# Optimization experiments

Hardware: AMD Instinct MI355X
Metric: run time of the kernel (lower is better)

The kernel has to match this reference:

```python
import jax, jax.numpy as jnp
import numpy as np

D_MODEL = 1024
NUM_HEADS = 16
HEAD_DIM = D_MODEL // NUM_HEADS


def setup_inputs() -> dict:
    key = jax.random.key(0)
    k1, k2, k3 = jax.random.split(key, 3)
    x = jax.random.normal(k1, (2, 2048, D_MODEL), dtype=jnp.float32)
    # trunc_normal init approximated by clipped normal with same std
    std_qkv = np.sqrt(2.0 / (D_MODEL + 3 * D_MODEL)).astype(np.float32)
    std_o = np.sqrt(2.0 / (D_MODEL + D_MODEL)).astype(np.float32)
    w_qkv = jnp.clip(jax.random.normal(k2, (3 * D_MODEL, D_MODEL), dtype=jnp.float32) * std_qkv,
                     -3 * std_qkv, 3 * std_qkv)
    w_o = jnp.clip(jax.random.normal(k3, (D_MODEL, D_MODEL), dtype=jnp.float32) * std_o,
                   -3 * std_o, 3 * std_o)
    return {"x": x, "w_qkv": w_qkv, "w_o": w_o}


def reference(x, w_qkv, w_o):
    b, s, d = x.shape
    h, hd = NUM_HEADS, HEAD_DIM
    # QKV projection: weight is [d_out, d_in]
    qkv = jnp.einsum('od,bsd->bso', w_qkv, x)  # [b, s, 3d]
    q, k, v = jnp.split(qkv, 3, axis=-1)
    # [b, s, d] -> [b, h, s, hd]
    def to_heads(t):
        return t.reshape(b, s, h, hd).transpose(0, 2, 1, 3)
    q_mh, k_mh, v_mh = to_heads(q), to_heads(k), to_heads(v)
    scale = 1.0 / jnp.sqrt(jnp.asarray(hd, dtype=x.dtype))
    scores = jnp.einsum('bhmd,bhnd->bhmn', q_mh, k_mh) * scale  # [b,h,s,s]
    causal = jnp.tril(jnp.ones((s, s), dtype=bool))
    scores = jnp.where(causal, scores, -jnp.inf)
    attn = jax.nn.softmax(scores, axis=-1)
    out = jnp.einsum('bhmn,bhnd->bhmd', attn, v_mh)  # [b,h,s,hd]
    out = out.transpose(0, 2, 1, 3).reshape(b, s, d)
    return jnp.einsum('od,bsd->bso', w_o, out)
```

## Files before the change

kernel.cpp:

```cpp
#include <hip/hip_runtime.h>

constexpr int SEQ = 2048;
constexpr int DM = 1024;
constexpr int NH = 16;
constexpr int BATCH = 2;
constexpr int MTOT = BATCH * SEQ;

typedef __bf16 bf16x8 __attribute__((ext_vector_type(8)));
typedef __bf16 bf16x4 __attribute__((ext_vector_type(4)));
typedef float f32x4 __attribute__((ext_vector_type(4)));

#define MFMA16(a, b, c) __builtin_amdgcn_mfma_f32_16x16x32_bf16((a), (b), (c), 0, 0, 0)

__device__ __forceinline__ void async_copy16(const void* g, void* l) {
  __builtin_amdgcn_global_load_lds((const __attribute__((address_space(1))) void*)g,
                                   (__attribute__((address_space(3))) void*)l, 16, 0, 0);
}

__global__ void sentinel_fill(float* out, int n) {
  int i = blockIdx.x * blockDim.x + threadIdx.x;
  for (; i < n; i += gridDim.x * blockDim.x) out[i] = 0.25f;
}

__global__ __launch_bounds__(256) void cvt_all(const float* __restrict__ x,
                                               const float* __restrict__ wq,
                                               const float* __restrict__ wo,
                                               __bf16* __restrict__ xb,
                                               __bf16* __restrict__ wqb,
                                               __bf16* __restrict__ wob) {
  const long i = (long)(blockIdx.x * 256 + threadIdx.x) * 8;
  const float* src;
  __bf16* dst;
  long off;
  if (i < 4194304) { src = x; dst = xb; off = i; }
  else if (i < 7340032) { src = wq; dst = wqb; off = i - 4194304; }
  else { src = wo; dst = wob; off = i - 7340032; }
  f32x4 lo = *(const f32x4*)(src + off);
  f32x4 hi = *(const f32x4*)(src + off + 4);
  bf16x8 r;
#pragma unroll
  for (int j = 0; j < 4; ++j) { r[j] = (__bf16)lo[j]; r[4 + j] = (__bf16)hi[j]; }
  *(bf16x8*)(dst + off) = r;
}

template <typename OutT>
__global__ __launch_bounds__(256) void gemm_bt(const __bf16* __restrict__ A,
                                               const __bf16* __restrict__ B,
                                               OutT* __restrict__ C,
                                               int M, int N, int K, int lda,
                                               float nanSig) {
  __shared__ alignas(16) __bf16 As[128 * 32];
  __shared__ alignas(16) __bf16 Bs[128 * 32];
  const int tid = threadIdx.x;
  const int lane = tid & 63;
  const int wave = tid >> 6;
  const int lr = lane & 15;
  const int quad = lane >> 4;
  const int wm = (wave >> 1) * 64;
  const int wn = (wave & 1) * 64;
  const int m0 = blockIdx.y * 128;
  const int n0 = blockIdx.x * 128;

  const int ra = tid >> 2;
  const int ca = (tid & 3) * 8;
  const __bf16* gA0 = A + (long)(m0 + ra) * lda + ca;
  const __bf16* gA1 = A + (long)(m0 + 64 + ra) * lda + ca;
  const __bf16* gB0 = B + (long)(n0 + ra) * K + ca;
  const __bf16* gB1 = B + (long)(n0 + 64 + ra) * K + ca;
  __bf16* lA0 = &As[wave * 512];
  __bf16* lA1 = &As[2048 + wave * 512];
  __bf16* lB0 = &Bs[wave * 512];
  __bf16* lB1 = &Bs[2048 + wave * 512];

  f32x4 acc[4][4];
#pragma unroll
  for (int i = 0; i < 4; ++i)
#pragma unroll
    for (int j = 0; j < 4; ++j) acc[i][j] = (f32x4){0.f, 0.f, 0.f, 0.f};

  for (int k0 = 0; k0 < K; k0 += 32) {
    async_copy16(gA0 + k0, lA0);
    async_copy16(gA1 + k0, lA1);
    async_copy16(gB0 + k0, lB0);
    async_copy16(gB1 + k0, lB1);
    __builtin_amdgcn_s_waitcnt(0);
    __syncthreads();
    bf16x8 af[4], bfr[4];
#pragma unroll
    for (int i = 0; i < 4; ++i) af[i] = *(const bf16x8*)&As[(wm + i * 16 + lr) * 32 + quad * 8];
#pragma unroll
    for (int j = 0; j < 4; ++j) bfr[j] = *(const bf16x8*)&Bs[(wn + j * 16 + lr) * 32 + quad * 8];
#pragma unroll
    for (int i = 0; i < 4; ++i)
#pragma unroll
      for (int j = 0; j < 4; ++j) acc[i][j] = MFMA16(af[i], bfr[j], acc[i][j]);
    __syncthreads();
  }

#pragma unroll
  for (int i = 0; i < 4; ++i) {
    const int row = m0 + wm + i * 16 + quad * 4;
#pragma unroll
    for (int j = 0; j < 4; ++j) {
      const int col = n0 + wn + j * 16 + lr;
#pragma unroll
      for (int r = 0; r < 4; ++r) {
        float v = acc[i][j][r];
        if (!(v == v)) v = nanSig;
        C[(long)(row + r) * N + col] = (OutT)v;
      }
    }
  }
}

template <int F32>
__device__ __forceinline__ bf16x8 load_cvt8(const void* base, long off) {
  if constexpr (F32) {
    const float* p = (const float*)base + off;
    f32x4 lo = *(const f32x4*)p;
    f32x4 hi = *(const f32x4*)(p + 4);
    bf16x8 r;
#pragma unroll
    for (int j = 0; j < 4; ++j) { r[j] = (__bf16)lo[j]; r[4 + j] = (__bf16)hi[j]; }
    return r;
  } else {
    return *(const bf16x8*)((const __bf16*)base + off);
  }
}

template <int AF32, int BF32, typename OutT>
__global__ __launch_bounds__(256) void gemm_nt(const void* __restrict__ Av,
                                               const void* __restrict__ Bv,
                                               OutT* __restrict__ C,
                                               int M, int N, int K, int lda,
                                               float nanSig) {
  __shared__ alignas(16) __bf16 As[128 * 32];
  __shared__ alignas(16) __bf16 Bs[128 * 32];
  const int tid = threadIdx.x;
  const int lane = tid & 63;
  const int wave = tid >> 6;
  const int lr = lane & 15;
  const int quad = lane >> 4;
  const int wm = (wave >> 1) * 64;
  const int wn = (wave & 1) * 64;
  const int m0 = blockIdx.y * 128;
  const int n0 = blockIdx.x * 128;

  const int r0 = tid >> 2;
  const int r1 = 64 + (tid >> 2);
  const int cc = (tid & 3) * 8;
  const long aBase0 = (long)(m0 + r0) * lda + cc;
  const long aBase1 = (long)(m0 + r1) * lda + cc;
  const long bBase0 = (long)(n0 + r0) * K + cc;
  const long bBase1 = (long)(n0 + r1) * K + cc;
  __bf16* lA0 = &As[r0 * 32 + cc];
  __bf16* lA1 = &As[r1 * 32 + cc];
  __bf16* lB0 = &Bs[r0 * 32 + cc];
  __bf16* lB1 = &Bs[r1 * 32 + cc];

  f32x4 acc[4][4];
#pragma unroll
  for (int i = 0; i < 4; ++i)
#pragma unroll
    for (int j = 0; j < 4; ++j) acc[i][j] = (f32x4){0.f, 0.f, 0.f, 0.f};

  for (int k0 = 0; k0 < K; k0 += 32) {
    bf16x8 va0 = load_cvt8<AF32>(Av, aBase0 + k0);
    bf16x8 va1 = load_cvt8<AF32>(Av, aBase1 + k0);
    bf16x8 vb0 = load_cvt8<BF32>(Bv, bBase0 + k0);
    bf16x8 vb1 = load_cvt8<BF32>(Bv, bBase1 + k0);
    __syncthreads();
    *(bf16x8*)lA0 = va0;
    *(bf16x8*)lA1 = va1;
    *(bf16x8*)lB0 = vb0;
    *(bf16x8*)lB1 = vb1;
    __syncthreads();
    bf16x8 af[4], bfr[4];
#pragma unroll
    for (int i = 0; i < 4; ++i) af[i] = *(const bf16x8*)&As[(wm + i * 16 + lr) * 32 + quad * 8];
#pragma unroll
    for (int j = 0; j < 4; ++j) bfr[j] = *(const bf16x8*)&Bs[(wn + j * 16 + lr) * 32 + quad * 8];
#pragma unroll
    for (int i = 0; i < 4; ++i)
#pragma unroll
      for (int j = 0; j < 4; ++j) acc[i][j] = MFMA16(af[i], bfr[j], acc[i][j]);
  }

#pragma unroll
  for (int i = 0; i < 4; ++i) {
    const int row = m0 + wm + i * 16 + quad * 4;
#pragma unroll
    for (int j = 0; j < 4; ++j) {
      const int col = n0 + wn + j * 16 + lr;
#pragma unroll
      for (int r = 0; r < 4; ++r) {
        float v = acc[i][j][r];
        if (!(v == v)) v = nanSig;
        C[(long)(row + r) * N + col] = (OutT)v;
      }
    }
  }
}

__global__ __launch_bounds__(256, 2) void attn_fwd(__bf16* __restrict__ qkv) {
  const int pi = blockIdx.x;
  const int h = blockIdx.y;
  const int b = blockIdx.z;
  const int q0A = pi * 64;
  const int q0B = (31 - pi) * 64;
  const int tid = threadIdx.x;
  const int lane = tid & 63;
  const int wave = tid >> 6;
  const int lr = lane & 15;
  const int quad = lane >> 4;
  const int wq = wave * 16;

  __shared__ alignas(16) __bf16 Ks[2][64 * 72];
  __shared__ alignas(16) __bf16 Vt[2][64 * 72];
  __shared__ alignas(16) __bf16 Pq[128 * 72];

  __bf16* pqw = &Pq[wave * 32 * 72];
  const long base = (long)b * SEQ * 3072;
  const int qi[2] = {q0A + wq + lr, q0B + wq + lr};

  bf16x8 b_q[2][2];
#pragma unroll
  for (int qg = 0; qg < 2; ++qg) {
    const long rowoff = base + (long)qi[qg] * 3072 + h * 64;
    b_q[qg][0] = *(const bf16x8*)(qkv + rowoff + quad * 8);
    b_q[qg][1] = *(const bf16x8*)(qkv + rowoff + 32 + quad * 8);
  }

  const float NEGS = -30000.f;
  const float SC = 0.18033688f;
  float m_i[2] = {NEGS, NEGS}, l_i[2] = {0.f, 0.f};
  f32x4 o_acc[2][4];
#pragma unroll
  for (int qg = 0; qg < 2; ++qg)
#pragma unroll
    for (int dt = 0; dt < 4; ++dt) o_acc[qg][dt] = (f32x4){0.f, 0.f, 0.f, 0.f};

  const int r_ = tid >> 3;
  const int col_ = (tid & 7) * 8;
  const int l8 = tid & 7;
  const int sw = (l8 & 3) << 3;
  const bool oddr = (tid >> 3) & 1;
  const int jb = oddr ? 4 : 0;

  const int T = 32 - pi;

  bf16x8 kreg[2], vreg[2];
  auto loadTile = [&](int t) {
    const long ro = base + ((long)t * 64 + r_) * 3072 + h * 64 + col_;
    kreg[0] = *(const bf16x8*)(qkv + ro + 1024);
    kreg[1] = *(const bf16x8*)(qkv + ro + (long)32 * 3072 + 1024);
    vreg[0] = *(const bf16x8*)(qkv + ro + 2048);
    vreg[1] = *(const bf16x8*)(qkv + ro + (long)32 * 3072 + 2048);
  };
  auto stageTile = [&](int bi) {
    __bf16* ks = &Ks[bi][0];
    __bf16* vt = &Vt[bi][0];
    *(bf16x8*)&ks[r_ * 72 + col_] = kreg[0];
    *(bf16x8*)&ks[(r_ + 32) * 72 + col_] = kreg[1];
#pragma unroll
    for (int c = 0; c < 2; ++c) {
      const int r = r_ + c * 32;
      const int rr = (r & ~1) ^ sw;
      int vd[4], od[4];
      __builtin_memcpy(vd, &vreg[c], 16);
#pragma unroll
      for (int i = 0; i < 4; ++i) od[i] = __shfl_xor(vd[i], 8);
#pragma unroll
      for (int i = 0; i < 4; ++i) {
        const int j = jb + i;
        const int a = vd[j >> 1], bb = od[j >> 1];
        const int lo = oddr ? bb : a;
        const int hi = oddr ? a : bb;
        const int pair = (j & 1) ? (int)(((unsigned)lo >> 16) | (hi & 0xffff0000))
                                 : (int)((lo & 0xffff) | (hi << 16));
        *(int*)&vt[(col_ + j) * 72 + rr] = pair;
      }
    }
  };

  loadTile(0);
  stageTile(0);
  loadTile(1);
  __syncthreads();

  for (int t = 0; t < T; ++t) {
    const int cur = t & 1;
    const int kv0 = t * 64;
    const bool actA = (kv0 <= q0A + wq + 15);

    f32x4 st[2][4];
#pragma unroll
    for (int kt = 0; kt < 4; ++kt) {
      st[1][kt] = (f32x4){0.f, 0.f, 0.f, 0.f};
      st[0][kt] = (f32x4){0.f, 0.f, 0.f, 0.f};
    }
    __builtin_amdgcn_s_setprio(1);
#pragma unroll
    for (int ks = 0; ks < 2; ++ks) {
      bf16x8 ak[4];
#pragma unroll
      for (int kt = 0; kt < 4; ++kt)
        ak[kt] = *(const bf16x8*)&Ks[cur][(kt * 16 + lr) * 72 + ks * 32 + quad * 8];
#pragma unroll
      for (int kt = 0; kt < 4; ++kt) st[1][kt] = MFMA16(ak[kt], b_q[1][ks], st[1][kt]);
      if (actA) {
#pragma unroll
        for (int kt = 0; kt < 4; ++kt) st[0][kt] = MFMA16(ak[kt], b_q[0][ks], st[0][kt]);
      }
    }
    __builtin_amdgcn_s_setprio(0);

    if (t + 1 < T) stageTile(cur ^ 1);
    if (t + 2 < T) loadTile(t + 2);

#pragma unroll
    for (int qg = 1; qg >= 0; --qg) {
      if (qg == 0 && !actA) continue;
      const int q0X = (qg == 0) ? q0A : q0B;
      if (kv0 + 64 <= q0X + wq) {
#pragma unroll
        for (int kt = 0; kt < 4; ++kt)
#pragma unroll
          for (int r = 0; r < 4; ++r) st[qg][kt][r] *= SC;
      } else {
#pragma unroll
        for (int kt = 0; kt < 4; ++kt) {
          const int d0 = kv0 + kt * 16 + quad * 4 - qi[qg];
#pragma unroll
          for (int r = 0; r < 4; ++r)
            st[qg][kt][r] = (d0 + r <= 0) ? st[qg][kt][r] * SC : NEGS;
        }
      }
      float mx = st[qg][0][0];
#pragma unroll
      for (int kt = 0; kt < 4; ++kt)
#pragma unroll
        for (int r = 0; r < 4; ++r) mx = fmaxf(mx, st[qg][kt][r]);
      mx = fmaxf(mx, __shfl_xor(mx, 16));
      mx = fmaxf(mx, __shfl_xor(mx, 32));
      const bool noresc = __all(mx - m_i[qg] <= 8.f);
      const float mnew = noresc ? m_i[qg] : fmaxf(m_i[qg], mx);
      float rs = 0.f;
#pragma unroll
      for (int kt = 0; kt < 4; ++kt)
#pragma unroll
        for (int r = 0; r < 4; ++r) {
          const float p = exp2f(st[qg][kt][r] - mnew);
          st[qg][kt][r] = p;
          rs += p;
        }
      rs += __shfl_xor(rs, 16);
      rs += __shfl_xor(rs, 32);
#pragma unroll
      for (int kt = 0; kt < 4; ++kt) {
        bf16x4 pv;
#pragma unroll
        for (int r = 0; r < 4; ++r) pv[r] = (__bf16)st[qg][kt][r];
        *(bf16x4*)&pqw[(qg * 16 + lr) * 72 + kt * 16 + quad * 4] = pv;
      }
      if (noresc) {
        l_i[qg] += rs;
      } else {
        const float alpha = exp2f(m_i[qg] - mnew);
        l_i[qg] = l_i[qg] * alpha + rs;
        m_i[qg] = mnew;
#pragma unroll
        for (int dt = 0; dt < 4; ++dt)
#pragma unroll
          for (int r = 0; r < 4; ++r) o_acc[qg][dt][r] *= alpha;
      }
    }

    asm volatile("s_waitcnt lgkmcnt(0)" ::: "memory");
    __builtin_amdgcn_sched_barrier(0);

    __builtin_amdgcn_s_setprio(1);
#pragma unroll
    for (int ks = 0; ks < 2; ++ks) {
      bf16x8 av[4];
#pragma unroll
      for (int dt = 0; dt < 4; ++dt) {
        const int blk = ((ks << 2) + quad) ^ ((2 * dt + (lr >> 3)) & 3);
        av[dt] = *(const bf16x8*)&Vt[cur][(dt * 16 + lr) * 72 + (blk << 3)];
      }
      {
        bf16x8 bp = *(const bf16x8*)&pqw[(16 + lr) * 72 + ks * 32 + quad * 8];
#pragma unroll
        for (int dt = 0; dt < 4; ++dt) o_acc[1][dt] = MFMA16(av[dt], bp, o_acc[1][dt]);
      }
      if (actA) {
        bf16x8 bp = *(const bf16x8*)&pqw[lr * 72 + ks * 32 + quad * 8];
#pragma unroll
        for (int dt = 0; dt < 4; ++dt) o_acc[0][dt] = MFMA16(av[dt], bp, o_acc[0][dt]);
      }
    }
    __builtin_amdgcn_s_setprio(0);

    __syncthreads();
  }

#pragma unroll
  for (int qg = 0; qg < 2; ++qg) {
    const float inv = 1.f / fmaxf(l_i[qg], 1e-30f);
    const long obase = base + (long)qi[qg] * 3072 + h * 64 + quad * 4;
#pragma unroll
    for (int dt = 0; dt < 4; ++dt) {
      bf16x4 ov;
#pragma unroll
      for (int r = 0; r < 4; ++r) ov[r] = (__bf16)(o_acc[qg][dt][r] * inv);
      *(bf16x4*)(qkv + obase + dt * 16) = ov;
    }
  }
}

extern "C" void kernel_launch(void* const* d_in, const int* in_sizes, int n_in,
                              void* d_out, int out_size, void* d_ws, size_t ws_size,
                              hipStream_t stream) {
  const float* x = (const float*)d_in[0];
  const float* w_qkv = (const float*)d_in[1];
  const float* w_o = (const float*)d_in[2];
  for (int i = 0; i < n_in; ++i) {
    if (in_sizes[i] == MTOT * DM) x = (const float*)d_in[i];
    else if (in_sizes[i] == 3 * DM * DM) w_qkv = (const float*)d_in[i];
    else if (in_sizes[i] == DM * DM) w_o = (const float*)d_in[i];
  }
  float* out = (float*)d_out;

  const size_t qkvBytes = (size_t)MTOT * 3072 * 2;
  const size_t xbBytes = (size_t)MTOT * DM * 2;
  const size_t wqBytes = (size_t)3 * DM * DM * 2;
  const size_t woBytes = (size_t)DM * DM * 2;
  const size_t needFast = qkvBytes + xbBytes + wqBytes + woBytes;

  __bf16* qkv = (__bf16*)d_ws;

  if (ws_size >= needFast) {
    __bf16* xb = (__bf16*)((char*)d_ws + qkvBytes);
    __bf16* wqb = (__bf16*)((char*)d_ws + qkvBytes + xbBytes);
    __bf16* wob = (__bf16*)((char*)d_ws + qkvBytes + xbBytes + wqBytes);
    cvt_all<<<4096, 256, 0, stream>>>(x, w_qkv, w_o, xb, wqb, wob);
    gemm_bt<__bf16><<<dim3(3072 / 128, MTOT / 128), 256, 0, stream>>>(
        xb, wqb, qkv, MTOT, 3072, DM, DM, 1e4f);
    attn_fwd<<<dim3(16, NH, BATCH), 256, 0, stream>>>(qkv);
    gemm_bt<float><<<dim3(DM / 128, MTOT / 128), 256, 0, stream>>>(
        qkv, wob, out, MTOT, DM, DM, 3072, 2e4f);
  } else if (ws_size >= qkvBytes) {
    gemm_nt<1, 1, __bf16><<<dim3(3072 / 128, MTOT / 128), 256, 0, stream>>>(
        x, w_qkv, qkv, MTOT, 3072, DM, DM, 1e4f);
    attn_fwd<<<dim3(16, NH, BATCH), 256, 0, stream>>>(qkv);
    gemm_nt<0, 1, float><<<dim3(DM / 128, MTOT / 128), 256, 0, stream>>>(
        qkv, w_o, out, MTOT, DM, DM, 3072, 2e4f);
  } else {
    sentinel_fill<<<256, 256, 0, stream>>>(out, out_size);
  }
}
```

Baseline: 231.7 us.

## Merge two query-pair blocks into one 512-thread block sharing K/V tiles

```diff
diff --git a/kernel.cpp b/kernel.cpp
--- a/kernel.cpp
+++ b/kernel.cpp
@@ -202,22 +202,24 @@
   }
 }
 
-__global__ __launch_bounds__(256, 2) void attn_fwd(__bf16* __restrict__ qkv) {
-  const int pi = blockIdx.x;
+__global__ __launch_bounds__(512, 2) void attn_fwd(__bf16* __restrict__ qkv) {
+  const int jj = blockIdx.x;
   const int h = blockIdx.y;
   const int b = blockIdx.z;
-  const int q0A = pi * 64;
-  const int q0B = (31 - pi) * 64;
   const int tid = threadIdx.x;
   const int lane = tid & 63;
   const int wave = tid >> 6;
+  const int ps = wave >> 2;
+  const int pi = 2 * jj + ps;
+  const int q0A = pi * 64;
+  const int q0B = (31 - pi) * 64;
   const int lr = lane & 15;
   const int quad = lane >> 4;
-  const int wq = wave * 16;
+  const int wq = (wave & 3) * 16;
 
   __shared__ alignas(16) __bf16 Ks[2][64 * 72];
   __shared__ alignas(16) __bf16 Vt[2][64 * 72];
-  __shared__ alignas(16) __bf16 Pq[128 * 72];
+  __shared__ alignas(16) __bf16 Pq[256 * 72];
 
   __bf16* pqw = &Pq[wave * 32 * 72];
   const long base = (long)b * SEQ * 3072;
@@ -247,39 +249,33 @@
   const bool oddr = (tid >> 3) & 1;
   const int jb = oddr ? 4 : 0;
 
-  const int T = 32 - pi;
-
-  bf16x8 kreg[2], vreg[2];
+  const int Tb = 32 - 2 * jj;
+  const int Tp = 32 - pi;
+
+  bf16x8 kreg, vreg;
   auto loadTile = [&](int t) {
     const long ro = base + ((long)t * 64 + r_) * 3072 + h * 64 + col_;
-    kreg[0] = *(const bf16x8*)(qkv + ro + 1024);
-    kreg[1] = *(const bf16x8*)(qkv + ro + (long)32 * 3072 + 1024);
-    vreg[0] = *(const bf16x8*)(qkv + ro + 2048);
-    vreg[1] = *(const bf16x8*)(qkv + ro + (long)32 * 3072 + 2048);
+    kreg = *(const bf16x8*)(qkv + ro + 1024);
+    vreg = *(const bf16x8*)(qkv + ro + 2048);
   };
   auto stageTile = [&](int bi) {
     __bf16* ks = &Ks[bi][0];
     __bf16* vt = &Vt[bi][0];
-    *(bf16x8*)&ks[r_ * 72 + col_] = kreg[0];
-    *(bf16x8*)&ks[(r_ + 32) * 72 + col_] = kreg[1];
-#pragma unroll
-    for (int c = 0; c < 2; ++c) {
-      const int r = r_ + c * 32;
-      const int rr = (r & ~1) ^ sw;
-      int vd[4], od[4];
-      __builtin_memcpy(vd, &vreg[c], 16);
-#pragma unroll
-      for (int i = 0; i < 4; ++i) od[i] = __shfl_xor(vd[i], 8);
-#pragma unroll
-      for (int i = 0; i < 4; ++i) {
-        const int j = jb + i;
-        const int a = vd[j >> 1], bb = od[j >> 1];
-        const int lo = oddr ? bb : a;
-        const int hi = oddr ? a : bb;
-        const int pair = (j & 1) ? (int)(((unsigned)lo >> 16) | (hi & 0xffff0000))
-                                 : (int)((lo & 0xffff) | (hi << 16));
-        *(int*)&vt[(col_ + j) * 72 + rr] = pair;
-      }
+    *(bf16x8*)&ks[r_ * 72 + col_] = kreg;
+    const int rr = (r_ & ~1) ^ sw;
+    int vd[4], od[4];
+    __builtin_memcpy(vd, &vreg, 16);
+#pragma unroll
+    for (int i = 0; i < 4; ++i) od[i] = __shfl_xor(vd[i], 8);
+#pragma unroll
+    for (int i = 0; i < 4; ++i) {
+      const int j = jb + i;
+      const int a = vd[j >> 1], bb = od[j >> 1];
+      const int lo = oddr ? bb : a;
+      const int hi = oddr ? a : bb;
+      const int pair = (j & 1) ? (int)(((unsigned)lo >> 16) | (hi & 0xffff0000))
+                               : (int)((lo & 0xffff) | (hi << 16));
+      *(int*)&vt[(col_ + j) * 72 + rr] = pair;
     }
   };
 
@@ -288,9 +284,10 @@
   loadTile(1);
   __syncthreads();
 
-  for (int t = 0; t < T; ++t) {
+  for (int t = 0; t < Tb; ++t) {
     const int cur = t & 1;
     const int kv0 = t * 64;
+    const bool active = (t < Tp);
     const bool actA = (kv0 <= q0A + wq + 15);
 
     f32x4 st[2][4];
@@ -299,107 +296,111 @@
       st[1][kt] = (f32x4){0.f, 0.f, 0.f, 0.f};
       st[0][kt] = (f32x4){0.f, 0.f, 0.f, 0.f};
     }
-    __builtin_amdgcn_s_setprio(1);
-#pragma unroll
-    for (int ks = 0; ks < 2; ++ks) {
-      bf16x8 ak[4];
-#pragma unroll
-      for (int kt = 0; kt < 4; ++kt)
-        ak[kt] = *(const bf16x8*)&Ks[cur][(kt * 16 + lr) * 72 + ks * 32 + quad * 8];
-#pragma unroll
-      for (int kt = 0; kt < 4; ++kt) st[1][kt] = MFMA16(ak[kt], b_q[1][ks], st[1][kt]);
-      if (actA) {
-#pragma unroll
-        for (int kt = 0; kt < 4; ++kt) st[0][kt] = MFMA16(ak[kt], b_q[0][ks], st[0][kt]);
+    if (active) {
+      __builtin_amdgcn_s_setprio(1);
+#pragma unroll
+      for (int ks = 0; ks < 2; ++ks) {
+        bf16x8 ak[4];
+#pragma unroll
+        for (int kt = 0; kt < 4; ++kt)
+          ak[kt] = *(const bf16x8*)&Ks[cur][(kt * 16 + lr) * 72 + ks * 32 + quad * 8];
+#pragma unroll
+        for (int kt = 0; kt < 4; ++kt) st[1][kt] = MFMA16(ak[kt], b_q[1][ks], st[1][kt]);
+        if (actA) {
+#pragma unroll
+          for (int kt = 0; kt < 4; ++kt) st[0][kt] = MFMA16(ak[kt], b_q[0][ks], st[0][kt]);
+        }
       }
-    }
-    __builtin_amdgcn_s_setprio(0);
-
-    if (t + 1 < T) stageTile(cur ^ 1);
-    if (t + 2 < T) loadTile(t + 2);
-
-#pragma unroll
-    for (int qg = 1; qg >= 0; --qg) {
-      if (qg == 0 && !actA) continue;
-      const int q0X = (qg == 0) ? q0A : q0B;
-      if (kv0 + 64 <= q0X + wq) {
+      __builtin_amdgcn_s_setprio(0);
+    }
+
+    if (t + 1 < Tb) stageTile(cur ^ 1);
+    if (t + 2 < Tb) loadTile(t + 2);
+
+    if (active) {
+#pragma unroll
+      for (int qg = 1; qg >= 0; --qg) {
+        if (qg == 0 && !actA) continue;
+        const int q0X = (qg == 0) ? q0A : q0B;
+        if (kv0 + 64 <= q0X + wq) {
+#pragma unroll
+          for (int kt = 0; kt < 4; ++kt)
+#pragma unroll
+            for (int r = 0; r < 4; ++r) st[qg][kt][r] *= SC;
+        } else {
+#pragma unroll
+          for (int kt = 0; kt < 4; ++kt) {
+            const int d0 = kv0 + kt * 16 + quad * 4 - qi[qg];
+#pragma unroll
+            for (int r = 0; r < 4; ++r)
+              st[qg][kt][r] = (d0 + r <= 0) ? st[qg][kt][r] * SC : NEGS;
+          }
+        }
+        float mx = st[qg][0][0];
 #pragma unroll
         for (int kt = 0; kt < 4; ++kt)
 #pragma unroll
-          for (int r = 0; r < 4; ++r) st[qg][kt][r] *= SC;
-      } else {
+          for (int r = 0; r < 4; ++r) mx = fmaxf(mx, st[qg][kt][r]);
+        mx = fmaxf(mx, __shfl_xor(mx, 16));
+        mx = fmaxf(mx, __shfl_xor(mx, 32));
+        const bool noresc = __all(mx - m_i[qg] <= 8.f);
+        const float mnew = noresc ? m_i[qg] : fmaxf(m_i[qg], mx);
+        float rs = 0.f;
+#pragma unroll
+        for (int kt = 0; kt < 4; ++kt)
+#pragma unroll
+          for (int r = 0; r < 4; ++r) {
+            const float p = exp2f(st[qg][kt][r] - mnew);
+            st[qg][kt][r] = p;
+            rs += p;
+          }
+        rs += __shfl_xor(rs, 16);
+        rs += __shfl_xor(rs, 32);
 #pragma unroll
         for (int kt = 0; kt < 4; ++kt) {
-          const int d0 = kv0 + kt * 16 + quad * 4 - qi[qg];
-#pragma unroll
-          for (int r = 0; r < 4; ++r)
-            st[qg][kt][r] = (d0 + r <= 0) ? st[qg][kt][r] * SC : NEGS;
+          bf16x4 pv;
+#pragma unroll
+          for (int r = 0; r < 4; ++r) pv[r] = (__bf16)st[qg][kt][r];
+          *(bf16x4*)&pqw[(qg * 16 + lr) * 72 + kt * 16 + quad * 4] = pv;
+        }
+        if (noresc) {
+          l_i[qg] += rs;
+        } else {
+          const float alpha = exp2f(m_i[qg] - mnew);
+          l_i[qg] = l_i[qg] * alpha + rs;
+          m_i[qg] = mnew;
+#pragma unroll
+          for (int dt = 0; dt < 4; ++dt)
+#pragma unroll
+            for (int r = 0; r < 4; ++r) o_acc[qg][dt][r] *= alpha;
         }
       }
-      float mx = st[qg][0][0];
-#pragma unroll
-      for (int kt = 0; kt < 4; ++kt)
-#pragma unroll
-        for (int r = 0; r < 4; ++r) mx = fmaxf(mx, st[qg][kt][r]);
-      mx = fmaxf(mx, __shfl_xor(mx, 16));
-      mx = fmaxf(mx, __shfl_xor(mx, 32));
-      const bool noresc = __all(mx - m_i[qg] <= 8.f);
-      const float mnew = noresc ? m_i[qg] : fmaxf(m_i[qg], mx);
-      float rs = 0.f;
-#pragma unroll
-      for (int kt = 0; kt < 4; ++kt)
-#pragma unroll
-        for (int r = 0; r < 4; ++r) {
-          const float p = exp2f(st[qg][kt][r] - mnew);
-          st[qg][kt][r] = p;
-          rs += p;
-        }
-      rs += __shfl_xor(rs, 16);
-      rs += __shfl_xor(rs, 32);
-#pragma unroll
-      for (int kt = 0; kt < 4; ++kt) {
-        bf16x4 pv;
-#pragma unroll
-        for (int r = 0; r < 4; ++r) pv[r] = (__bf16)st[qg][kt][r];
-        *(bf16x4*)&pqw[(qg * 16 + lr) * 72 + kt * 16 + quad * 4] = pv;
+
+      asm volatile("s_waitcnt lgkmcnt(0)" ::: "memory");
+      __builtin_amdgcn_sched_barrier(0);
+
+      __builtin_amdgcn_s_setprio(1);
+#pragma unroll
+      for (int ks = 0; ks < 2; ++ks) {
+        bf16x8 av[4];
+#pragma unroll
+        for (int dt = 0; dt < 4; ++dt) {
+          const int blk = ((ks << 2) + quad) ^ ((2 * dt + (lr >> 3)) & 3);
+          av[dt] = *(const bf16x8*)&Vt[cur][(dt * 16 + lr) * 72 + (blk << 3)];
+        }
+        {
+          bf16x8 bp = *(const bf16x8*)&pqw[(16 + lr) * 72 + ks * 32 + quad * 8];
+#pragma unroll
+          for (int dt = 0; dt < 4; ++dt) o_acc[1][dt] = MFMA16(av[dt], bp, o_acc[1][dt]);
+        }
+        if (actA) {
+          bf16x8 bp = *(const bf16x8*)&pqw[lr * 72 + ks * 32 + quad * 8];
+#pragma unroll
+          for (int dt = 0; dt < 4; ++dt) o_acc[0][dt] = MFMA16(av[dt], bp, o_acc[0][dt]);
+        }
       }
-      if (noresc) {
-        l_i[qg] += rs;
-      } else {
-        const float alpha = exp2f(m_i[qg] - mnew);
-        l_i[qg] = l_i[qg] * alpha + rs;
-        m_i[qg] = mnew;
-#pragma unroll
-        for (int dt = 0; dt < 4; ++dt)
-#pragma unroll
-          for (int r = 0; r < 4; ++r) o_acc[qg][dt][r] *= alpha;
-      }
-    }
-
-    asm volatile("s_waitcnt lgkmcnt(0)" ::: "memory");
-    __builtin_amdgcn_sched_barrier(0);
-
-    __builtin_amdgcn_s_setprio(1);
-#pragma unroll
-    for (int ks = 0; ks < 2; ++ks) {
-      bf16x8 av[4];
-#pragma unroll
-      for (int dt = 0; dt < 4; ++dt) {
-        const int blk = ((ks << 2) + quad) ^ ((2 * dt + (lr >> 3)) & 3);
-        av[dt] = *(const bf16x8*)&Vt[cur][(dt * 16 + lr) * 72 + (blk << 3)];
-      }
-      {
-        bf16x8 bp = *(const bf16x8*)&pqw[(16 + lr) * 72 + ks * 32 + quad * 8];
-#pragma unroll
-        for (int dt = 0; dt < 4; ++dt) o_acc[1][dt] = MFMA16(av[dt], bp, o_acc[1][dt]);
-      }
-      if (actA) {
-        bf16x8 bp = *(const bf16x8*)&pqw[lr * 72 + ks * 32 + quad * 8];
-#pragma unroll
-        for (int dt = 0; dt < 4; ++dt) o_acc[0][dt] = MFMA16(av[dt], bp, o_acc[0][dt]);
-      }
-    }
-    __builtin_amdgcn_s_setprio(0);
+      __builtin_amdgcn_s_setprio(0);
+    }
 
     __syncthreads();
   }
@@ -446,13 +447,13 @@
     cvt_all<<<4096, 256, 0, stream>>>(x, w_qkv, w_o, xb, wqb, wob);
     gemm_bt<__bf16><<<dim3(3072 / 128, MTOT / 128), 256, 0, stream>>>(
         xb, wqb, qkv, MTOT, 3072, DM, DM, 1e4f);
-    attn_fwd<<<dim3(16, NH, BATCH), 256, 0, stream>>>(qkv);
+    attn_fwd<<<dim3(8, NH, BATCH), 512, 0, stream>>>(qkv);
     gemm_bt<float><<<dim3(DM / 128, MTOT / 128), 256, 0, stream>>>(
         qkv, wob, out, MTOT, DM, DM, 3072, 2e4f);
   } else if (ws_size >= qkvBytes) {
     gemm_nt<1, 1, __bf16><<<dim3(3072 / 128, MTOT / 128), 256, 0, stream>>>(
         x, w_qkv, qkv, MTOT, 3072, DM, DM, 1e4f);
-    attn_fwd<<<dim3(16, NH, BATCH), 256, 0, stream>>>(qkv);
+    attn_fwd<<<dim3(8, NH, BATCH), 512, 0, stream>>>(qkv);
     gemm_nt<0, 1, float><<<dim3(DM / 128, MTOT / 128), 256, 0, stream>>>(
         qkv, w_o, out, MTOT, DM, DM, 3072, 2e4f);
   } else {
```

Result: faster. 216.3 us (-6.6%).
